# Optimization experiments

Hardware: AMD Instinct MI355X
Metric: run time of the kernel (lower is better)

## Reference

```python
import jax, jax.numpy as jnp
import numpy as np

B, D, H, T, F = 2, 256, 8, 128, 64
C = H * F          # channels = 512
TE = 512           # time_embed_dim


def setup_inputs() -> dict:
    key = jax.random.key(0)
    ks = jax.random.split(key, 9)
    pd = jax.random.randint(ks[2], (B, T, T), 0, 2 * T - 1, dtype=jnp.int32) - (T - 1)
    s = 0.02
    return {
        "qk": jax.random.normal(ks[0], (B, D, H, T, F), jnp.float32),
        "temb": jax.random.normal(ks[1], (B, T, TE), jnp.float32),
        "pairwise_distances": pd,
        "w_dist": jax.random.normal(ks[3], (3, C), jnp.float32) * s,
        "b_dist": jax.random.normal(ks[4], (C,), jnp.float32) * s,
        "w_time": jax.random.normal(ks[5], (TE, C), jnp.float32) * s,
        "b_time": jax.random.normal(ks[6], (C,), jnp.float32) * s,
        "w_out": jax.random.normal(ks[7], (C, C), jnp.float32) * s,
        "b_out": jax.random.normal(ks[8], (C,), jnp.float32) * s,
    }


def _rpe_net(temb, pd, w_dist, b_dist, w_time, b_time, w_out, b_out):
    d = pd.astype(jnp.float32)
    # (B, T, S, 3): log(1+d+), log(1+d-), indicator(d==0)
    dist_embs = jnp.stack(
        [jnp.log1p(jnp.maximum(d, 0.0)),
         jnp.log1p(jnp.maximum(-d, 0.0)),
         (pd == 0).astype(jnp.float32)],
        axis=-1,
    )
    emb = (temb @ w_time + b_time)[:, :, None, :] + dist_embs @ w_dist + b_dist  # (B,T,S,C)
    R = jax.nn.silu(emb) @ w_out + b_out  # (B,T,S,C)
    return R.reshape(*pd.shape, H, F)     # (B,T,S,H,F)


def reference(qk, temb, pairwise_distances, w_dist, b_dist, w_time, b_time, w_out, b_out):
    R = _rpe_net(temb, pairwise_distances, w_dist, b_dist, w_time, b_time, w_out, b_out)
    # forward_qk: contract head_dim f for every (t, s) pair
    return jnp.einsum('bdhtf,btshf->bdhts', qk, R)
```

## Files before the change

kernel.cpp:

```cpp
#include <hip/hip_runtime.h>
#include <hip/hip_bf16.h>

#define B_  2
#define D_  256
#define H_  8
#define T_  128
#define S_  128
#define F_  64
#define C_  512
#define TE_ 512

typedef _Float16 f16x8 __attribute__((ext_vector_type(8)));
typedef _Float16 f16x4 __attribute__((ext_vector_type(4)));
typedef float    f32x4 __attribute__((ext_vector_type(4)));

__global__ __launch_bounds__(256) void k_time_proj(
    const float* __restrict__ temb, const float* __restrict__ w_time,
    const float* __restrict__ b_time, const float* __restrict__ b_dist,
    float* __restrict__ tp)
{
    int row0 = blockIdx.x * 2;
    int tid  = threadIdx.x;
    __shared__ float te[2][TE_];
    for (int i = tid; i < 2 * TE_; i += 256)
        te[i >> 9][i & 511] = temb[(size_t)row0 * TE_ + i];
    __syncthreads();
    for (int half = 0; half < 2; ++half) {
        int c = tid + half * 256;
        float bias = b_time[c] + b_dist[c];
        float a0 = bias, a1 = bias;
        for (int e = 0; e < TE_; ++e) {
            float w = w_time[(size_t)e * C_ + c];
            a0 += te[0][e] * w;
            a1 += te[1][e] * w;
        }
        tp[(size_t)row0 * C_ + c]       = a0;
        tp[(size_t)(row0 + 1) * C_ + c] = a1;
    }
}

__global__ __launch_bounds__(128) void k_embed_silu(
    const float* __restrict__ tp, const int* __restrict__ pd,
    const float* __restrict__ w_dist, _Float16* __restrict__ A)
{
    int row = blockIdx.x;
    int bt  = row >> 7;
    int d   = pd[row];
    float f0 = log1pf(fmaxf((float)d, 0.f));
    float f1 = log1pf(fmaxf((float)(-d), 0.f));
    float f2 = (d == 0) ? 1.f : 0.f;
    int c0 = threadIdx.x * 4;
    float4 t4 = *(const float4*)&tp[(size_t)bt * C_ + c0];
    float4 w0 = *(const float4*)&w_dist[c0];
    float4 w1 = *(const float4*)&w_dist[C_ + c0];
    float4 w2 = *(const float4*)&w_dist[2 * C_ + c0];
    float e0 = t4.x + f0 * w0.x + f1 * w1.x + f2 * w2.x;
    float e1 = t4.y + f0 * w0.y + f1 * w1.y + f2 * w2.y;
    float e2 = t4.z + f0 * w0.z + f1 * w1.z + f2 * w2.z;
    float e3 = t4.w + f0 * w0.w + f1 * w1.w + f2 * w2.w;
    f16x4 v;
    v.x = (_Float16)(e0 / (1.f + expf(-e0)));
    v.y = (_Float16)(e1 / (1.f + expf(-e1)));
    v.z = (_Float16)(e2 / (1.f + expf(-e2)));
    v.w = (_Float16)(e3 / (1.f + expf(-e3)));
    *(f16x4*)&A[(size_t)row * C_ + c0] = v;
}

__global__ __launch_bounds__(512) void k_wt(
    const float* __restrict__ w_out, _Float16* __restrict__ Wt)
{
    int n = blockIdx.x;
    int k = threadIdx.x;
    Wt[(size_t)n * C_ + k] = (_Float16)w_out[(size_t)k * C_ + n];
}

__global__ __launch_bounds__(256) void k_gemm_R(
    const _Float16* __restrict__ A, const _Float16* __restrict__ Wt,
    const float* __restrict__ b_out, _Float16* __restrict__ R)
{
    const int K = 512, N = 512;
    __shared__ _Float16 As[128][72];
    __shared__ _Float16 Bs[128][72];
    int bm = blockIdx.x, bn = blockIdx.y;
    int tid = threadIdx.x;
    int wave = tid >> 6, lane = tid & 63;
    int wm = (wave >> 1) * 64, wn = (wave & 1) * 64;
    int mrow = lane & 15, kq = (lane >> 4) * 8;
    int lrow = tid >> 3, lcol = (tid & 7) * 8;
    const size_t arow0 = (size_t)bm * 128;
    f32x4 acc[4][4] = {};
    for (int k0 = 0; k0 < K; k0 += 64) {
#pragma unroll
        for (int p = 0; p < 4; ++p) {
            int r = p * 32 + lrow;
            *(f16x8*)&As[r][lcol] = *(const f16x8*)&A[(arow0 + r) * K + k0 + lcol];
            *(f16x8*)&Bs[r][lcol] = *(const f16x8*)&Wt[(size_t)(bn * 128 + r) * K + k0 + lcol];
        }
        __syncthreads();
#pragma unroll
        for (int ks = 0; ks < 64; ks += 32) {
            f16x8 af[4], bfr[4];
#pragma unroll
            for (int i = 0; i < 4; ++i) af[i]  = *(const f16x8*)&As[wm + i * 16 + mrow][ks + kq];
#pragma unroll
            for (int j = 0; j < 4; ++j) bfr[j] = *(const f16x8*)&Bs[wn + j * 16 + mrow][ks + kq];
#pragma unroll
            for (int i = 0; i < 4; ++i)
#pragma unroll
                for (int j = 0; j < 4; ++j)
                    acc[i][j] = __builtin_amdgcn_mfma_f32_16x16x32_f16(af[i], bfr[j], acc[i][j], 0, 0, 0);
        }
        __syncthreads();
    }
    int col = lane & 15, rb = (lane >> 4) * 4;
#pragma unroll
    for (int j = 0; j < 4; ++j) {
        int n = bn * 128 + wn + j * 16 + col;
        float bo = b_out[n];
#pragma unroll
        for (int i = 0; i < 4; ++i)
#pragma unroll
            for (int r = 0; r < 4; ++r) {
                size_t m = arow0 + wm + i * 16 + rb + r;
                R[m * N + n] = (_Float16)(acc[i][j][r] + bo);
            }
    }
}

__global__ __launch_bounds__(256) void k_einsum(
    const float* __restrict__ qk, const _Float16* __restrict__ R,
    float* __restrict__ out)
{
    __shared__ _Float16 Aq[128][72];
    __shared__ _Float16 Br[128][72];
    int bht  = blockIdx.x;
    int dblk = blockIdx.y;
    int t = bht & 127;
    int h = (bht >> 7) & 7;
    int b = bht >> 10;
    int tid = threadIdx.x;
    int wave = tid >> 6, lane = tid & 63;
    int wm = (wave >> 1) * 64, wn = (wave & 1) * 64;

    const size_t qbase = (size_t)b * (D_ * H_ * T_ * F_) + (size_t)h * (T_ * F_)
                       + (size_t)t * F_ + (size_t)dblk * 128 * (H_ * T_ * F_);
    {
        int r  = tid >> 4;
        int c4 = (tid & 15) * 4;
#pragma unroll
        for (int p = 0; p < 8; ++p) {
            int row = p * 16 + r;
            float4 v = *(const float4*)&qk[qbase + (size_t)row * (H_ * T_ * F_) + c4];
            f16x4 hv;
            hv.x = (_Float16)v.x; hv.y = (_Float16)v.y;
            hv.z = (_Float16)v.z; hv.w = (_Float16)v.w;
            *(f16x4*)&Aq[row][c4] = hv;
        }
    }
    {
        const size_t rbase = ((size_t)(b * T_ + t) * S_) * C_ + h * 64;
        int r  = tid >> 3;
        int c8 = (tid & 7) * 8;
#pragma unroll
        for (int p = 0; p < 4; ++p) {
            int row = p * 32 + r;
            *(f16x8*)&Br[row][c8] = *(const f16x8*)&R[rbase + (size_t)row * C_ + c8];
        }
    }
    __syncthreads();

    int mrow = lane & 15, kq = (lane >> 4) * 8;
    f32x4 acc[4][4] = {};
#pragma unroll
    for (int ks = 0; ks < 64; ks += 32) {
        f16x8 af[4], bfr[4];
#pragma unroll
        for (int i = 0; i < 4; ++i) af[i]  = *(const f16x8*)&Aq[wm + i * 16 + mrow][ks + kq];
#pragma unroll
        for (int j = 0; j < 4; ++j) bfr[j] = *(const f16x8*)&Br[wn + j * 16 + mrow][ks + kq];
#pragma unroll
        for (int i = 0; i < 4; ++i)
#pragma unroll
            for (int j = 0; j < 4; ++j)
                acc[i][j] = __builtin_amdgcn_mfma_f32_16x16x32_f16(af[i], bfr[j], acc[i][j], 0, 0, 0);
    }

    const size_t obase = (size_t)b * (D_ * H_ * T_ * S_) + (size_t)h * (T_ * S_)
                       + (size_t)t * S_ + (size_t)dblk * 128 * (H_ * T_ * S_);
    int col = lane & 15, rb = (lane >> 4) * 4;
#pragma unroll
    for (int i = 0; i < 4; ++i)
#pragma unroll
        for (int r = 0; r < 4; ++r) {
            int dloc = wm + i * 16 + rb + r;
            size_t o = obase + (size_t)dloc * (H_ * T_ * S_);
#pragma unroll
            for (int j = 0; j < 4; ++j)
                out[o + wn + j * 16 + col] = acc[i][j][r];
        }
}

extern "C" void kernel_launch(void* const* d_in, const int* in_sizes, int n_in,
                              void* d_out, int out_size, void* d_ws, size_t ws_size,
                              hipStream_t stream) {
    (void)in_sizes; (void)n_in; (void)out_size; (void)ws_size;
    const float* qk     = (const float*)d_in[0];
    const float* temb   = (const float*)d_in[1];
    const int*   pd     = (const int*)d_in[2];
    const float* w_dist = (const float*)d_in[3];
    const float* b_dist = (const float*)d_in[4];
    const float* w_time = (const float*)d_in[5];
    const float* b_time = (const float*)d_in[6];
    const float* w_out  = (const float*)d_in[7];
    const float* b_out  = (const float*)d_in[8];
    float* out = (float*)d_out;

    char* ws = (char*)d_ws;
    float*     tp = (float*)ws;
    _Float16*  Wt = (_Float16*)(ws + 512 * 1024);
    _Float16*  A  = (_Float16*)(ws + 1024 * 1024);
    _Float16*  R  = (_Float16*)(ws + 1024 * 1024 + 33554432);

    k_time_proj<<<dim3(B_ * T_ / 2), dim3(256), 0, stream>>>(temb, w_time, b_time, b_dist, tp);
    k_wt<<<dim3(C_), dim3(C_), 0, stream>>>(w_out, Wt);
    k_embed_silu<<<dim3(B_ * T_ * S_), dim3(128), 0, stream>>>(tp, pd, w_dist, A);
    k_gemm_R<<<dim3(256, 4), dim3(256), 0, stream>>>(A, Wt, b_out, R);
    k_einsum<<<dim3(B_ * H_ * T_, 2), dim3(256), 0, stream>>>(qk, R, out);
}
```

Measured before the change: 509.4 us.

## Load einsum operands directly to registers, use global_load_lds in GEMM, vectorize time projection

The einsum kernel no longer stages qk and R through shared memory. Each lane loads its MFMA fragments straight from global memory, swaps operands so each lane holds four consecutive s outputs, and writes them as float4 stores instead of scattered scalar stores. The R GEMM now uses global_load_lds direct-to-LDS loads with an unpadded tile, which may bring back LDS bank conflicts. The time projection is reworked to one row per block with float4 weight loads.

After: 512.4 us. Within noise of the previous version (+0.6%).

```diff
diff --git a/kernel.cpp b/kernel.cpp
--- a/kernel.cpp
+++ b/kernel.cpp
@@ -14,29 +14,39 @@
 typedef _Float16 f16x4 __attribute__((ext_vector_type(4)));
 typedef float    f32x4 __attribute__((ext_vector_type(4)));
 
-__global__ __launch_bounds__(256) void k_time_proj(
+#define AS1 __attribute__((address_space(1)))
+#define AS3 __attribute__((address_space(3)))
+
+__global__ __launch_bounds__(128) void k_time_proj(
     const float* __restrict__ temb, const float* __restrict__ w_time,
     const float* __restrict__ b_time, const float* __restrict__ b_dist,
     float* __restrict__ tp)
 {
-    int row0 = blockIdx.x * 2;
-    int tid  = threadIdx.x;
-    __shared__ float te[2][TE_];
-    for (int i = tid; i < 2 * TE_; i += 256)
-        te[i >> 9][i & 511] = temb[(size_t)row0 * TE_ + i];
+    int row = blockIdx.x;
+    int tid = threadIdx.x;
+    __shared__ float te[TE_];
+    for (int i = tid; i < TE_; i += 128)
+        te[i] = temb[(size_t)row * TE_ + i];
     __syncthreads();
-    for (int half = 0; half < 2; ++half) {
-        int c = tid + half * 256;
-        float bias = b_time[c] + b_dist[c];
-        float a0 = bias, a1 = bias;
-        for (int e = 0; e < TE_; ++e) {
-            float w = w_time[(size_t)e * C_ + c];
-            a0 += te[0][e] * w;
-            a1 += te[1][e] * w;
-        }
-        tp[(size_t)row0 * C_ + c]       = a0;
-        tp[(size_t)(row0 + 1) * C_ + c] = a1;
-    }
+    int c0 = tid * 4;
+    float4 b0 = *(const float4*)&b_time[c0];
+    float4 b1 = *(const float4*)&b_dist[c0];
+    float ax0 = 0.f, ay0 = 0.f, az0 = 0.f, aw0 = 0.f;
+    float ax1 = 0.f, ay1 = 0.f, az1 = 0.f, aw1 = 0.f;
+#pragma unroll 4
+    for (int e = 0; e < TE_; e += 2) {
+        float s0 = te[e], s1 = te[e + 1];
+        float4 w0 = *(const float4*)&w_time[(size_t)e * C_ + c0];
+        float4 w1 = *(const float4*)&w_time[(size_t)(e + 1) * C_ + c0];
+        ax0 += s0 * w0.x; ay0 += s0 * w0.y; az0 += s0 * w0.z; aw0 += s0 * w0.w;
+        ax1 += s1 * w1.x; ay1 += s1 * w1.y; az1 += s1 * w1.z; aw1 += s1 * w1.w;
+    }
+    float4 r;
+    r.x = b0.x + b1.x + ax0 + ax1;
+    r.y = b0.y + b1.y + ay0 + ay1;
+    r.z = b0.z + b1.z + az0 + az1;
+    r.w = b0.w + b1.w + aw0 + aw1;
+    *(float4*)&tp[(size_t)row * C_ + c0] = r;
 }
 
 __global__ __launch_bounds__(128) void k_embed_silu(
@@ -79,22 +89,28 @@
     const float* __restrict__ b_out, _Float16* __restrict__ R)
 {
     const int K = 512, N = 512;
-    __shared__ _Float16 As[128][72];
-    __shared__ _Float16 Bs[128][72];
+    __shared__ _Float16 As[128][64];
+    __shared__ _Float16 Bs[128][64];
     int bm = blockIdx.x, bn = blockIdx.y;
     int tid = threadIdx.x;
     int wave = tid >> 6, lane = tid & 63;
     int wm = (wave >> 1) * 64, wn = (wave & 1) * 64;
     int mrow = lane & 15, kq = (lane >> 4) * 8;
-    int lrow = tid >> 3, lcol = (tid & 7) * 8;
+    int grow = lane >> 3;
+    int gcol = (lane & 7) * 8;
     const size_t arow0 = (size_t)bm * 128;
+    const size_t brow0 = (size_t)bn * 128;
     f32x4 acc[4][4] = {};
     for (int k0 = 0; k0 < K; k0 += 64) {
 #pragma unroll
         for (int p = 0; p < 4; ++p) {
-            int r = p * 32 + lrow;
-            *(f16x8*)&As[r][lcol] = *(const f16x8*)&A[(arow0 + r) * K + k0 + lcol];
-            *(f16x8*)&Bs[r][lcol] = *(const f16x8*)&Wt[(size_t)(bn * 128 + r) * K + k0 + lcol];
+            int rb = (p * 4 + wave) * 8;
+            __builtin_amdgcn_global_load_lds(
+                (const AS1 void*)(const void*)&A[(arow0 + rb + grow) * K + k0 + gcol],
+                (AS3 void*)(void*)&As[rb][0], 16, 0, 0);
+            __builtin_amdgcn_global_load_lds(
+                (const AS1 void*)(const void*)&Wt[(brow0 + rb + grow) * K + k0 + gcol],
+                (AS3 void*)(void*)&Bs[rb][0], 16, 0, 0);
         }
         __syncthreads();
 #pragma unroll
@@ -131,8 +147,6 @@
     const float* __restrict__ qk, const _Float16* __restrict__ R,
     float* __restrict__ out)
 {
-    __shared__ _Float16 Aq[128][72];
-    __shared__ _Float16 Br[128][72];
     int bht  = blockIdx.x;
     int dblk = blockIdx.y;
     int t = bht & 127;
@@ -141,63 +155,50 @@
     int tid = threadIdx.x;
     int wave = tid >> 6, lane = tid & 63;
     int wm = (wave >> 1) * 64, wn = (wave & 1) * 64;
-
+    int mrow = lane & 15, kq = (lane >> 4) * 8;
+
+    const size_t qstr  = (size_t)(H_ * T_ * F_);
     const size_t qbase = (size_t)b * (D_ * H_ * T_ * F_) + (size_t)h * (T_ * F_)
-                       + (size_t)t * F_ + (size_t)dblk * 128 * (H_ * T_ * F_);
-    {
-        int r  = tid >> 4;
-        int c4 = (tid & 15) * 4;
-#pragma unroll
-        for (int p = 0; p < 8; ++p) {
-            int row = p * 16 + r;
-            float4 v = *(const float4*)&qk[qbase + (size_t)row * (H_ * T_ * F_) + c4];
-            f16x4 hv;
-            hv.x = (_Float16)v.x; hv.y = (_Float16)v.y;
-            hv.z = (_Float16)v.z; hv.w = (_Float16)v.w;
-            *(f16x4*)&Aq[row][c4] = hv;
+                       + (size_t)t * F_ + (size_t)dblk * 128 * qstr;
+    const size_t rbase = ((size_t)(b * T_ + t) * S_) * C_ + h * 64;
+
+    f32x4 acc[4][4] = {};
+#pragma unroll
+    for (int ks = 0; ks < 64; ks += 32) {
+        f16x8 bf[4], aq[4];
+#pragma unroll
+        for (int j = 0; j < 4; ++j)
+            bf[j] = *(const f16x8*)&R[rbase + (size_t)(wn + j * 16 + mrow) * C_ + ks + kq];
+#pragma unroll
+        for (int i = 0; i < 4; ++i) {
+            const float* qp = &qk[qbase + (size_t)(wm + i * 16 + mrow) * qstr + ks + kq];
+            float4 u = *(const float4*)qp;
+            float4 v = *(const float4*)(qp + 4);
+            f16x8 a;
+            a[0] = (_Float16)u.x; a[1] = (_Float16)u.y;
+            a[2] = (_Float16)u.z; a[3] = (_Float16)u.w;
+            a[4] = (_Float16)v.x; a[5] = (_Float16)v.y;
+            a[6] = (_Float16)v.z; a[7] = (_Float16)v.w;
+            aq[i] = a;
         }
-    }
-    {
-        const size_t rbase = ((size_t)(b * T_ + t) * S_) * C_ + h * 64;
-        int r  = tid >> 3;
-        int c8 = (tid & 7) * 8;
-#pragma unroll
-        for (int p = 0; p < 4; ++p) {
-            int row = p * 32 + r;
-            *(f16x8*)&Br[row][c8] = *(const f16x8*)&R[rbase + (size_t)row * C_ + c8];
-        }
-    }
-    __syncthreads();
-
-    int mrow = lane & 15, kq = (lane >> 4) * 8;
-    f32x4 acc[4][4] = {};
-#pragma unroll
-    for (int ks = 0; ks < 64; ks += 32) {
-        f16x8 af[4], bfr[4];
-#pragma unroll
-        for (int i = 0; i < 4; ++i) af[i]  = *(const f16x8*)&Aq[wm + i * 16 + mrow][ks + kq];
-#pragma unroll
-        for (int j = 0; j < 4; ++j) bfr[j] = *(const f16x8*)&Br[wn + j * 16 + mrow][ks + kq];
-#pragma unroll
-        for (int i = 0; i < 4; ++i)
-#pragma unroll
-            for (int j = 0; j < 4; ++j)
-                acc[i][j] = __builtin_amdgcn_mfma_f32_16x16x32_f16(af[i], bfr[j], acc[i][j], 0, 0, 0);
-    }
-
+#pragma unroll
+        for (int j = 0; j < 4; ++j)
+#pragma unroll
+            for (int i = 0; i < 4; ++i)
+                acc[j][i] = __builtin_amdgcn_mfma_f32_16x16x32_f16(bf[j], aq[i], acc[j][i], 0, 0, 0);
+    }
+
+    const size_t ostr  = (size_t)(H_ * T_ * S_);
     const size_t obase = (size_t)b * (D_ * H_ * T_ * S_) + (size_t)h * (T_ * S_)
-                       + (size_t)t * S_ + (size_t)dblk * 128 * (H_ * T_ * S_);
-    int col = lane & 15, rb = (lane >> 4) * 4;
-#pragma unroll
-    for (int i = 0; i < 4; ++i)
-#pragma unroll
-        for (int r = 0; r < 4; ++r) {
-            int dloc = wm + i * 16 + rb + r;
-            size_t o = obase + (size_t)dloc * (H_ * T_ * S_);
-#pragma unroll
-            for (int j = 0; j < 4; ++j)
-                out[o + wn + j * 16 + col] = acc[i][j][r];
-        }
+                       + (size_t)t * S_ + (size_t)dblk * 128 * ostr;
+    int dcol = lane & 15, sb = (lane >> 4) * 4;
+#pragma unroll
+    for (int i = 0; i < 4; ++i) {
+        size_t orow = obase + (size_t)(wm + i * 16 + dcol) * ostr + wn + sb;
+#pragma unroll
+        for (int j = 0; j < 4; ++j)
+            *(f32x4*)&out[orow + j * 16] = acc[j][i];
+    }
 }
 
 extern "C" void kernel_launch(void* const* d_in, const int* in_sizes, int n_in,
@@ -221,7 +222,7 @@
     _Float16*  A  = (_Float16*)(ws + 1024 * 1024);
     _Float16*  R  = (_Float16*)(ws + 1024 * 1024 + 33554432);
 
-    k_time_proj<<<dim3(B_ * T_ / 2), dim3(256), 0, stream>>>(temb, w_time, b_time, b_dist, tp);
+    k_time_proj<<<dim3(B_ * T_), dim3(128), 0, stream>>>(temb, w_time, b_time, b_dist, tp);
     k_wt<<<dim3(C_), dim3(C_), 0, stream>>>(w_out, Wt);
     k_embed_silu<<<dim3(B_ * T_ * S_), dim3(128), 0, stream>>>(tp, pd, w_dist, A);
     k_gemm_R<<<dim3(256, 4), dim3(256), 0, stream>>>(A, Wt, b_out, R);
```
